# Performance work log

Measured on AMD Instinct MI355X. Metric: run time of the kernel, lower is better.

The kernel has to match this reference:

```python
import jax, jax.numpy as jnp
import numpy as np

BN_EPS = 1e-5

def setup_inputs() -> dict:
    key = jax.random.key(0)
    k1, k2, k3, k4 = jax.random.split(key, 4)
    B, V, DI, DO = 4096, 64, 128, 128
    feat = jax.random.normal(k1, (B, V, DI), dtype=jnp.float32)
    adj = jax.random.uniform(k2, (V, V), dtype=jnp.float32)
    # per-vertex Linear weights (stacked): W[v] maps dim_in -> dim_out
    W = jax.random.normal(k3, (V, DI, DO), dtype=jnp.float32) * (1.0 / np.sqrt(DI))
    b = jax.random.normal(k4, (V, DO), dtype=jnp.float32) * 0.01
    gamma = jnp.ones((V, DO), dtype=jnp.float32)
    beta = jnp.zeros((V, DO), dtype=jnp.float32)
    return {"feat": feat, "adj": adj, "W": W, "b": b, "gamma": gamma, "beta": beta}

def reference(feat, adj, W, b, gamma, beta):
    # Per-vertex Linear as one grouped GEMM: [B,V,DI] x [V,DI,DO] -> [B,V,DO]
    h = jnp.einsum('bvi,vio->bvo', feat, W) + b[None, :, :]
    # BatchNorm1d (training mode): normalize over batch dim, per vertex & channel
    mu = jnp.mean(h, axis=0, keepdims=True)            # [1,V,DO]
    var = jnp.mean((h - mu) ** 2, axis=0, keepdims=True)  # biased variance
    h = (h - mu) * jax.lax.rsqrt(var + BN_EPS) * gamma[None] + beta[None]
    # adjacency mix: adj [V,V] applied to every batch element, then relu
    out = jnp.einsum('uv,bvo->buo', adj, h)
    return jax.nn.relu(out)
```

## Files before the change

kernel.cpp:

```cpp
#include <hip/hip_runtime.h>

#define BN 4096
#define VN 64
#define DI 128
#define DO 128

typedef __attribute__((ext_vector_type(8))) short short8;
typedef __attribute__((ext_vector_type(4))) float f32x4;

__device__ __forceinline__ float bf2f(unsigned short s) {
    return __uint_as_float(((unsigned)s) << 16);
}
__device__ __forceinline__ unsigned short f2bf(float f) {
    unsigned u = __float_as_uint(f);
    u += 0x7FFF + ((u >> 16) & 1);
    return (unsigned short)(u >> 16);
}
__device__ __forceinline__ unsigned pack_bf16_trunc(float lo, float hi) {
    return __builtin_amdgcn_perm(__float_as_uint(hi), __float_as_uint(lo), 0x07060302u);
}
__device__ __forceinline__ unsigned pack_bf16_rne(float lo, float hi) {
    return (unsigned)f2bf(lo) | ((unsigned)f2bf(hi) << 16);
}


__global__ __launch_bounds__(256) void k_prep(const float* __restrict__ W,
                                              const float* __restrict__ adj,
                                              unsigned short* __restrict__ Wt,
                                              unsigned short* __restrict__ adjbf) {
    const int t = threadIdx.x, blk = blockIdx.x;
    if (blk < 512) {
        const int v = blk >> 3, q = blk & 7;
        const float* Wv = W + (size_t)v * DI * DO;
        unsigned short* Wtv = Wt + (size_t)v * DI * DO;
        const int o = t & 127;
        const int i0 = q * 16 + (t >> 7) * 8;
        short8 s0;
#pragma unroll
        for (int j = 0; j < 8; ++j)
            s0[j] = (short)f2bf(Wv[(size_t)(i0 + j) * DO + o]);
        *(short8*)(Wtv + o * DI + i0) = s0;
    } else {
        short8 s0, s1;
#pragma unroll
        for (int j = 0; j < 8; ++j) s0[j] = (short)f2bf(adj[t * 16 + j]);
#pragma unroll
        for (int j = 0; j < 8; ++j) s1[j] = (short)f2bf(adj[t * 16 + 8 + j]);
        *(short8*)(adjbf + t * 16) = s0;
        *(short8*)(adjbf + t * 16 + 8) = s1;
    }
}

__global__ __launch_bounds__(256) void k_gemm1(const float* __restrict__ feat,
                                               const unsigned short* __restrict__ Wt,
                                               const float* __restrict__ bias,
                                               unsigned short* __restrict__ h,
                                               float* __restrict__ psA,
                                               float* __restrict__ psB) {
    const int v = blockIdx.x;
    const int bt = blockIdx.y;
    const int tid = threadIdx.x;
    const int w = tid >> 6, lane = tid & 63;
    const int wm = w >> 1, wn = w & 1;
    const int quad = lane >> 4, l16 = lane & 15;

    size_t aidx[4];
#pragma unroll
    for (int rt = 0; rt < 4; ++rt)
        aidx[rt] = (size_t)(bt * 128 + wm * 64 + rt * 16 + l16) * (VN * DI)
                 + v * DI + quad * 8;

    short8 bb[4][4];
#pragma unroll
    for (int ks = 0; ks < 4; ++ks)
#pragma unroll
        for (int nt = 0; nt < 4; ++nt)
            bb[ks][nt] = *(const short8*)(Wt + (size_t)v * (DI * DO)
                                          + (size_t)(wn * 64 + nt * 16 + l16) * DI
                                          + quad * 8 + ks * 32);

    f32x4 acc[4][4];
#pragma unroll
    for (int rt = 0; rt < 4; ++rt)
#pragma unroll
        for (int nt = 0; nt < 4; ++nt) acc[rt][nt] = (f32x4){0.f, 0.f, 0.f, 0.f};

#define LOADA(dst, k0)                                                        \
    {                                                                         \
        _Pragma("unroll") for (int rt = 0; rt < 4; ++rt) {                    \
            f32x4 f0 = *(const f32x4*)(feat + aidx[rt] + (k0));               \
            f32x4 f1 = *(const f32x4*)(feat + aidx[rt] + (k0) + 4);          \
            union { short8 s; unsigned u[4]; } pk;                            \
            pk.u[0] = pack_bf16_trunc(f0[0], f0[1]);                          \
            pk.u[1] = pack_bf16_trunc(f0[2], f0[3]);                          \
            pk.u[2] = pack_bf16_trunc(f1[0], f1[1]);                          \
            pk.u[3] = pack_bf16_trunc(f1[2], f1[3]);                          \
            dst[rt] = pk.s;                                                   \
        }                                                                     \
    }

    short8 aCur[4], aNxt[4];
    LOADA(aCur, 0)
#pragma unroll
    for (int ks = 0; ks < 4; ++ks) {
        if (ks < 3) LOADA(aNxt, (ks + 1) * 32)
#pragma unroll
        for (int rt = 0; rt < 4; ++rt)
#pragma unroll
            for (int nt = 0; nt < 4; ++nt)
                acc[rt][nt] = __builtin_amdgcn_mfma_f32_16x16x32_bf16(
                    aCur[rt], bb[ks][nt], acc[rt][nt], 0, 0, 0);
#pragma unroll
        for (int rt = 0; rt < 4; ++rt) aCur[rt] = aNxt[rt];
    }
#undef LOADA

    unsigned short* hblk = h + ((size_t)(bt * 64 + v) * 4 + w) * 4096;
#pragma unroll
    for (int nt = 0; nt < 4; ++nt) {
        const int col = wn * 64 + nt * 16 + l16;
        const float bv = bias[v * DO + col];
        float s = 0.f, sq = 0.f;
#pragma unroll
        for (int rt = 0; rt < 4; ++rt)
#pragma unroll
            for (int e = 0; e < 4; ++e) {
                float x = acc[rt][nt][e] + bv;
                acc[rt][nt][e] = x;
                s += x;
                sq += x * x;
            }
        s += __shfl_down(s, 32);  s += __shfl_down(s, 16);
        sq += __shfl_down(sq, 32); sq += __shfl_down(sq, 16);
        if (lane < 16) {
            const size_t pi = ((size_t)(v * 32 + bt) * 2 + wm) * 128 + col;
            psA[pi] = s;
            psB[pi] = sq;
        }
#pragma unroll
        for (int rt = 0; rt < 4; ++rt) {
            uint2 pk;
            pk.x = pack_bf16_rne(acc[rt][nt][0], acc[rt][nt][1]);
            pk.y = pack_bf16_rne(acc[rt][nt][2], acc[rt][nt][3]);
            *(uint2*)(hblk + (size_t)((nt * 4 + rt) * 64 + lane) * 4) = pk;
        }
    }
}

__global__ __launch_bounds__(128) void k_reduce(const float* __restrict__ psA,
                                                const float* __restrict__ psB,
                                                const float* __restrict__ gamma,
                                                const float* __restrict__ beta,
                                                float* __restrict__ scale,
                                                float* __restrict__ shift) {
    const int o = threadIdx.x;
    const int v = blockIdx.x;
    float s = 0.f, sq = 0.f;
#pragma unroll
    for (int p = 0; p < 64; ++p) {
        const size_t pi = ((size_t)v * 64 + p) * 128 + o;
        s += psA[pi];
        sq += psB[pi];
    }
    const float invB = 1.0f / (float)BN;
    const float mu = s * invB;
    const float var = sq * invB - mu * mu;
    const float sc = gamma[v * DO + o] * rsqrtf(var + 1e-5f);
    scale[v * DO + o] = sc;
    shift[v * DO + o] = beta[v * DO + o] - mu * sc;
}

__global__ __launch_bounds__(128) void k_c0(const float* __restrict__ adj,
                                            const float* __restrict__ shift,
                                            float* __restrict__ C0) {
    const int o = threadIdx.x;
    const int u = blockIdx.x;
    float c0 = 0.f;
#pragma unroll
    for (int v = 0; v < VN; ++v)
        c0 += adj[u * VN + v] * shift[v * DO + o];
    C0[u * DO + o] = c0;
}

__global__ __launch_bounds__(512, 4) void k_mix(const unsigned short* __restrict__ h,
                                                const float* __restrict__ scale,
                                                const unsigned short* __restrict__ adjbf,
                                                const float* __restrict__ C0,
                                                float* __restrict__ out) {
    __shared__ unsigned short hsT[4][DO][72];
    const int t = threadIdx.x;
    const int b0 = blockIdx.x * 4;
    const int bt = b0 >> 7;
    const int r = b0 & 127;
    const int swm = r >> 6, srt = (r >> 4) & 3, squad = (r >> 2) & 3;

#pragma unroll
    for (int c = 0; c < 16; ++c) {
        const int p = c * 512 + t;
        const int v = p >> 7, o = p & 127;
        const size_t off = (size_t)(bt * 64 + v) * 16384
                         + (size_t)(((swm * 2 + (o >> 6)) * 4 + ((o >> 4) & 3)) * 4 + srt) * 256
                         + (size_t)(squad * 16 + (o & 15)) * 4;
        const uint2 pk = *(const uint2*)(h + off);
        const float sc = scale[v * DO + o];
        hsT[0][o][v] = f2bf(bf2f((unsigned short)(pk.x & 0xFFFF)) * sc);
        hsT[1][o][v] = f2bf(bf2f((unsigned short)(pk.x >> 16)) * sc);
        hsT[2][o][v] = f2bf(bf2f((unsigned short)(pk.y & 0xFFFF)) * sc);
        hsT[3][o][v] = f2bf(bf2f((unsigned short)(pk.y >> 16)) * sc);
    }
    __syncthreads();

    const int w = t >> 6, lane = t & 63;
    const int bl = w >> 1, nh = w & 1;
    const int quad = lane >> 4, l16 = lane & 15;
    const int b = b0 + bl;

    short8 af[4][2];
#pragma unroll
    for (int mt = 0; mt < 4; ++mt)
#pragma unroll
        for (int ks = 0; ks < 2; ++ks)
            af[mt][ks] = *(const short8*)(adjbf + (mt * 16 + l16) * VN
                                          + ks * 32 + quad * 8);

    f32x4 acc[4][4];
#pragma unroll
    for (int mt = 0; mt < 4; ++mt)
#pragma unroll
        for (int nt = 0; nt < 4; ++nt) acc[mt][nt] = (f32x4){0.f, 0.f, 0.f, 0.f};

#pragma unroll
    for (int nt = 0; nt < 4; ++nt) {
        const unsigned short* bp = &hsT[bl][nh * 64 + nt * 16 + l16][quad * 8];
        short8 bf0 = *(const short8*)(bp);
        short8 bf1 = *(const short8*)(bp + 32);
#pragma unroll
        for (int mt = 0; mt < 4; ++mt) {
            acc[mt][nt] = __builtin_amdgcn_mfma_f32_16x16x32_bf16(
                af[mt][0], bf0, acc[mt][nt], 0, 0, 0);
            acc[mt][nt] = __builtin_amdgcn_mfma_f32_16x16x32_bf16(
                af[mt][1], bf1, acc[mt][nt], 0, 0, 0);
        }
    }

#pragma unroll
    for (int mt = 0; mt < 4; ++mt)
#pragma unroll
        for (int nt = 0; nt < 4; ++nt) {
            const int o = nh * 64 + nt * 16 + l16;
#pragma unroll
            for (int e = 0; e < 4; ++e) {
                const int u = mt * 16 + quad * 4 + e;
                out[((size_t)b * VN + u) * DO + o] =
                    fmaxf(acc[mt][nt][e] + C0[u * DO + o], 0.0f);
            }
        }
}

extern "C" void kernel_launch(void* const* d_in, const int* in_sizes, int n_in,
                              void* d_out, int out_size, void* d_ws, size_t ws_size,
                              hipStream_t stream) {
    const float* feat  = (const float*)d_in[0];
    const float* adj   = (const float*)d_in[1];
    const float* W     = (const float*)d_in[2];
    const float* bias  = (const float*)d_in[3];
    const float* gamma = (const float*)d_in[4];
    const float* beta  = (const float*)d_in[5];
    float* out = (float*)d_out;

    char* ws = (char*)d_ws;
    unsigned short* h     = (unsigned short*)ws;
    unsigned short* Wt    = (unsigned short*)(ws + 67108864ull);
    unsigned short* adjbf = (unsigned short*)(ws + 69206016ull);
    float* psA   = (float*)(ws + 69214208ull);
    float* psB   = psA + 524288;
    float* scale = psB + 524288;
    float* shift = scale + 8192;
    float* C0    = shift + 8192;

    k_prep<<<dim3(513), dim3(256), 0, stream>>>(W, adj, Wt, adjbf);
    k_gemm1<<<dim3(64, 32), dim3(256), 0, stream>>>(feat, Wt, bias, h, psA, psB);
    k_reduce<<<dim3(64), dim3(128), 0, stream>>>(psA, psB, gamma, beta, scale, shift);
    k_c0<<<dim3(64), dim3(128), 0, stream>>>(adj, shift, C0);
    k_mix<<<dim3(1024), dim3(512), 0, stream>>>(h, scale, adjbf, C0, out);
}
```

Before: 297.7 us.

## Stage feature tile into LDS via direct global-to-LDS loads with XOR swizzle

The GEMM1 kernel now loads the whole 128x128 fp32 feature tile for each (vertex, batch-tile) block into shared memory using global_load_lds, with an XOR swizzle on 16-byte chunks, and then reads MFMA A fragments from LDS. Before, each wave issued scattered 32-byte global reads per row, two wave-row groups fetched the same A rows, and loads were software-pipelined. The aim is fully coalesced 512-byte row fetches and no duplicate global traffic. In exchange the kernel uses 64KB of LDS, which limits occupancy, and a block barrier now separates the load phase from the compute phase.

```diff
diff --git a/kernel.cpp b/kernel.cpp
--- a/kernel.cpp
+++ b/kernel.cpp
@@ -57,6 +57,7 @@
                                                unsigned short* __restrict__ h,
                                                float* __restrict__ psA,
                                                float* __restrict__ psB) {
+    __shared__ float ldsA[128 * 128];
     const int v = blockIdx.x;
     const int bt = blockIdx.y;
     const int tid = threadIdx.x;
@@ -64,56 +65,62 @@
     const int wm = w >> 1, wn = w & 1;
     const int quad = lane >> 4, l16 = lane & 15;
 
-    size_t aidx[4];
+    const unsigned short* wbase = Wt + (size_t)v * (DI * DO)
+                                + (size_t)(wn * 64 + l16) * DI + quad * 8;
+    short8 bb[4][4];
+#pragma unroll
+    for (int ks = 0; ks < 4; ++ks)
+#pragma unroll
+        for (int nt = 0; nt < 4; ++nt)
+            bb[ks][nt] = *(const short8*)(wbase + nt * (16 * DI) + ks * 32);
+
+    {
+        const int lrow = lane >> 5;
+        const int lpos = lane & 31;
+#pragma unroll
+        for (int i = 0; i < 16; ++i) {
+            const int row = w * 32 + 2 * i + lrow;
+            const int gchunk = lpos ^ (row & 7);
+            const float* src = feat + (size_t)(bt * 128 + row) * (VN * DI)
+                             + v * DI + gchunk * 4;
+            float* dst = &ldsA[(w * 32 + 2 * i) * 128];
+            __builtin_amdgcn_global_load_lds(
+                (const __attribute__((address_space(1))) void*)src,
+                (__attribute__((address_space(3))) void*)dst, 16, 0, 0);
+        }
+    }
+    __syncthreads();
+
+    f32x4 acc[4][4];
 #pragma unroll
     for (int rt = 0; rt < 4; ++rt)
-        aidx[rt] = (size_t)(bt * 128 + wm * 64 + rt * 16 + l16) * (VN * DI)
-                 + v * DI + quad * 8;
-
-    short8 bb[4][4];
-#pragma unroll
-    for (int ks = 0; ks < 4; ++ks)
-#pragma unroll
-        for (int nt = 0; nt < 4; ++nt)
-            bb[ks][nt] = *(const short8*)(Wt + (size_t)v * (DI * DO)
-                                          + (size_t)(wn * 64 + nt * 16 + l16) * DI
-                                          + quad * 8 + ks * 32);
-
-    f32x4 acc[4][4];
-#pragma unroll
-    for (int rt = 0; rt < 4; ++rt)
 #pragma unroll
         for (int nt = 0; nt < 4; ++nt) acc[rt][nt] = (f32x4){0.f, 0.f, 0.f, 0.f};
 
-#define LOADA(dst, k0)                                                        \
-    {                                                                         \
-        _Pragma("unroll") for (int rt = 0; rt < 4; ++rt) {                    \
-            f32x4 f0 = *(const f32x4*)(feat + aidx[rt] + (k0));               \
-            f32x4 f1 = *(const f32x4*)(feat + aidx[rt] + (k0) + 4);          \
-            union { short8 s; unsigned u[4]; } pk;                            \
-            pk.u[0] = pack_bf16_trunc(f0[0], f0[1]);                          \
-            pk.u[1] = pack_bf16_trunc(f0[2], f0[3]);                          \
-            pk.u[2] = pack_bf16_trunc(f1[0], f1[1]);                          \
-            pk.u[3] = pack_bf16_trunc(f1[2], f1[3]);                          \
-            dst[rt] = pk.s;                                                   \
-        }                                                                     \
-    }
-
-    short8 aCur[4], aNxt[4];
-    LOADA(aCur, 0)
 #pragma unroll
     for (int ks = 0; ks < 4; ++ks) {
-        if (ks < 3) LOADA(aNxt, (ks + 1) * 32)
+        short8 aCur[4];
+#pragma unroll
+        for (int rt = 0; rt < 4; ++rt) {
+            const int row = wm * 64 + rt * 16 + l16;
+            const int xr = row & 7;
+            const int c0 = ks * 8 + quad * 2;
+            const f32x4 f0 = *(const f32x4*)&ldsA[row * 128 + ((c0    ) ^ xr) * 4];
+            const f32x4 f1 = *(const f32x4*)&ldsA[row * 128 + ((c0 + 1) ^ xr) * 4];
+            union { short8 s; unsigned u[4]; } pk;
+            pk.u[0] = pack_bf16_trunc(f0[0], f0[1]);
+            pk.u[1] = pack_bf16_trunc(f0[2], f0[3]);
+            pk.u[2] = pack_bf16_trunc(f1[0], f1[1]);
+            pk.u[3] = pack_bf16_trunc(f1[2], f1[3]);
+            aCur[rt] = pk.s;
+        }
 #pragma unroll
         for (int rt = 0; rt < 4; ++rt)
 #pragma unroll
             for (int nt = 0; nt < 4; ++nt)
                 acc[rt][nt] = __builtin_amdgcn_mfma_f32_16x16x32_bf16(
                     aCur[rt], bb[ks][nt], acc[rt][nt], 0, 0, 0);
-#pragma unroll
-        for (int rt = 0; rt < 4; ++rt) aCur[rt] = aNxt[rt];
-    }
-#undef LOADA
+    }
 
     unsigned short* hblk = h + ((size_t)(bt * 64 + v) * 4 + w) * 4096;
 #pragma unroll
```

Result: faster. 286.1 us (-3.9%).
